# Performance work log

Hardware: AMD Instinct MI355X
Metric: run time of the kernel (lower is better)

## Reference

```python
import jax, jax.numpy as jnp
import numpy as np
import math

DIM_IN = 512
DIM_OUT = 512
KERNEL = 3
STYLE_DIM = 2 * 128
LIN_SCALE = 1.0 / math.sqrt(STYLE_DIM)      # EqualLinear scale (lr_mul=1)
CONV_SCALE = 1.0 / math.sqrt(DIM_IN * KERNEL ** 2)  # fan_in = dim_in * k**2 (as in source)
PAD = KERNEL // 2


def setup_inputs() -> dict:
    key = jax.random.key(0)
    ks = jax.random.split(key, 5)
    B, T = 16, 2048
    x = jax.random.normal(ks[0], (B, DIM_IN, T), dtype=jnp.float32)
    c_src = jax.random.normal(ks[1], (B, 128), dtype=jnp.float32)
    c_trg = jax.random.normal(ks[2], (B, 128), dtype=jnp.float32)
    style_w = jax.random.normal(ks[3], (DIM_IN, STYLE_DIM), dtype=jnp.float32)
    style_b = jnp.ones((DIM_IN,), dtype=jnp.float32)  # bias_init=1
    weight = jax.random.normal(ks[4], (1, DIM_OUT, DIM_IN, KERNEL), dtype=jnp.float32)
    return {"x": x, "c_src": c_src, "c_trg": c_trg,
            "style_w": style_w, "style_b": style_b, "weight": weight}


def reference(x, c_src, c_trg, style_w, style_b, weight):
    B = x.shape[0]
    # EqualLinear: style code s [B, dim_in]
    c = jnp.concatenate([c_src, c_trg], axis=-1)              # [B, 256]
    s = c @ (style_w * LIN_SCALE).T + style_b                 # [B, dim_in]
    # Modulate: w [B, dim_out, dim_in, k]
    w = CONV_SCALE * weight * s[:, None, :, None]
    # Demodulate over (dim_in, k)
    demod = jax.lax.rsqrt(jnp.sum(w * w, axis=(2, 3)) + 1e-8)  # [B, dim_out]
    w = w * demod[:, :, None, None]
    # Per-sample conv1d, padding 'same' (pad = k//2), vmapped over batch
    def conv1(xi, wi):
        # xi: [dim_in, T], wi: [dim_out, dim_in, k]
        out = jax.lax.conv_general_dilated(
            xi[None], wi, window_strides=(1,), padding=[(PAD, PAD)],
            dimension_numbers=("NCH", "OIH", "NCH"))
        return out[0]                                          # [dim_out, T]
    return jax.vmap(conv1)(x, w)                               # [B, dim_out, T]
```

## Files before the change

kernel.cpp:

```cpp
#include <hip/hip_runtime.h>
#include <cstdint>
#include <cstddef>


#define LIN_SCALE  0.0625f
#define CONV_SCALE 0.014731391f

#define B_   16
#define CIN  512
#define COUT 512
#define T_   2048
#define TP   2050

typedef __bf16 bf16x8 __attribute__((ext_vector_type(8)));
typedef float  f32x4  __attribute__((ext_vector_type(4)));
typedef unsigned short u16x8 __attribute__((ext_vector_type(8)));
typedef unsigned short u16x2 __attribute__((ext_vector_type(2)));

#define AS1 __attribute__((address_space(1)))
#define AS3 __attribute__((address_space(3)))

__device__ inline unsigned short f2bf(float f) {
  __bf16 h = (__bf16)f;
  return __builtin_bit_cast(unsigned short, h);
}

__global__ __launch_bounds__(256) void style_kernel(const float* __restrict__ c_src,
                                                    const float* __restrict__ c_trg,
                                                    const float* __restrict__ sw,
                                                    const float* __restrict__ sb,
                                                    float* __restrict__ s) {
  __shared__ float c[256];
  const int b = blockIdx.y;
  const int tid = threadIdx.x;
  c[tid] = (tid < 128) ? c_src[b * 128 + tid] : c_trg[b * 128 + tid - 128];
  __syncthreads();
  const int w = tid >> 6, lane = tid & 63;
  #pragma unroll
  for (int rr = 0; rr < 16; ++rr) {
    const int i = blockIdx.x * 64 + w * 16 + rr;
    const float* row = sw + (size_t)i * 256;
    float acc = row[lane] * c[lane] + row[lane + 64] * c[lane + 64]
              + row[lane + 128] * c[lane + 128] + row[lane + 192] * c[lane + 192];
    #pragma unroll
    for (int off = 32; off; off >>= 1) acc += __shfl_down(acc, off, 64);
    if (lane == 0) s[b * 512 + i] = acc * LIN_SCALE + sb[i];
  }
}

__global__ __launch_bounds__(256) void fused_prep_kernel(const float* __restrict__ x,
                                                         const float* __restrict__ s,
                                                         const float* __restrict__ weight,
                                                         unsigned short* __restrict__ xT,
                                                         float* __restrict__ demod,
                                                         unsigned short* __restrict__ Wb) {
  __shared__ __align__(16) char smem[16896];
  const int id  = blockIdx.x;
  const int tid = threadIdx.x;

  if (id < 4096) {
    float* tile = (float*)smem;
    float* ss   = (float*)(smem + 16640);
    const int t0 = (id & 31) * 64;
    const int i0 = ((id >> 5) & 7) * 64;
    const int b  = id >> 8;

    if (tid < 64) ss[tid] = s[(size_t)b * 512 + i0 + tid];

    const int lr = tid >> 4;
    const int lc = (tid & 15) * 4;
    const float* xb = x + ((size_t)b * CIN + i0) * T_ + t0;
    #pragma unroll
    for (int p = 0; p < 4; ++p) {
      const int r = p * 16 + lr;
      const float4 v = *(const float4*)(xb + (size_t)r * T_ + lc);
      tile[r * 65 + lc + 0] = v.x; tile[r * 65 + lc + 1] = v.y;
      tile[r * 65 + lc + 2] = v.z; tile[r * 65 + lc + 3] = v.w;
    }
    if (t0 == 0 && tid < 8)
      *(u16x8*)&xT[(size_t)b * TP * CIN + i0 + tid * 8] = (u16x8){0,0,0,0,0,0,0,0};
    if (t0 == T_ - 64 && tid < 8)
      *(u16x8*)&xT[((size_t)b * TP + TP - 1) * CIN + i0 + tid * 8] = (u16x8){0,0,0,0,0,0,0,0};
    __syncthreads();

    const int st = tid >> 3;
    const int si = (tid & 7) * 8;
    float sv[8];
    #pragma unroll
    for (int q = 0; q < 8; ++q) sv[q] = ss[si + q];
    unsigned short* xTb = xT + ((size_t)b * TP + 1 + t0) * CIN + i0;
    #pragma unroll
    for (int p = 0; p < 2; ++p) {
      const int t = p * 32 + st;
      u16x8 v;
      #pragma unroll
      for (int q = 0; q < 8; ++q) v[q] = f2bf(tile[(si + q) * 65 + t] * sv[q]);
      *(u16x8*)&xTb[(size_t)t * CIN + si] = v;
    }
  } else {
    const int o = id - 4096;
    float* wsh     = (float*)smem;
    float* partial = (float*)(smem + 6144);

    #pragma unroll
    for (int j = tid; j < 384; j += 256)
      ((float4*)wsh)[j] = ((const float4*)(weight + (size_t)o * 1536))[j];
    __syncthreads();

    float wr[6];
    #pragma unroll
    for (int q = 0; q < 6; ++q) wr[q] = wsh[tid * 6 + q] * CONV_SCALE;

    #pragma unroll
    for (int k = 0; k < 3; ++k) {
      u16x2 v;
      v.x = f2bf(wr[k]);
      v.y = f2bf(wr[3 + k]);
      *(u16x2*)&Wb[((size_t)(k * 512 + o)) * 512 + 2 * tid] = v;
    }

    float s0v[16], s1v[16];
    #pragma unroll
    for (int b = 0; b < 16; ++b) {
      s0v[b] = s[b * 512 + 2 * tid];
      s1v[b] = s[b * 512 + 2 * tid + 1];
    }

    const int lane = tid & 63, w = tid >> 6;
    float ssb[16];
    #pragma unroll
    for (int b = 0; b < 16; ++b) {
      float ssq = 0.f;
      #pragma unroll
      for (int q = 0; q < 3; ++q) { float v = wr[q] * s0v[b]; ssq += v * v; }
      #pragma unroll
      for (int q = 3; q < 6; ++q) { float v = wr[q] * s1v[b]; ssq += v * v; }
      ssb[b] = ssq;
    }
    #pragma unroll
    for (int b = 0; b < 16; ++b) {
      float ssq = ssb[b];
      #pragma unroll
      for (int off = 32; off; off >>= 1) ssq += __shfl_down(ssq, off, 64);
      if (lane == 0) partial[b * 4 + w] = ssq;
    }
    __syncthreads();
    if (tid < 16)
      demod[(size_t)tid * 512 + o] =
          rsqrtf(partial[tid * 4] + partial[tid * 4 + 1] + partial[tid * 4 + 2]
               + partial[tid * 4 + 3] + 1e-8f);
  }
}

__global__ __launch_bounds__(256, 2) void gemm_kernel(const unsigned short* __restrict__ Wb,
                                                      const unsigned short* __restrict__ xT,
                                                      const float* __restrict__ demod,
                                                      float* __restrict__ out) {
  __shared__ unsigned short lA[3 * 128 * 32];
  __shared__ unsigned short lB[258 * 32];

  const int id  = blockIdx.x;
  const int xcd = id & 7;
  const int j   = id >> 3;
  const int b   = xcd + 8 * (j >> 5);
  const int r   = j & 31;
  const int o0  = (r >> 3) * 128;
  const int t0  = (r & 7) * 256;

  const int tid  = threadIdx.x;
  const int lane = tid & 63;
  const int wm   = ((tid >> 6) & 1) * 64;
  const int wn   = (tid >> 7) * 128;
  const int rl   = lane & 15;
  const int kc   = lane >> 4;

  const unsigned short* gW = Wb + (size_t)o0 * 512;
  const unsigned short* gX = xT + ((size_t)b * TP + t0) * CIN;

  f32x4 acc[8][4];
  #pragma unroll
  for (int i = 0; i < 8; ++i)
    #pragma unroll
    for (int jj = 0; jj < 4; ++jj) acc[i][jj] = (f32x4){0.f, 0.f, 0.f, 0.f};

  for (int kk = 0; kk < 16; ++kk) {
    const int i0 = kk * 32;
    __syncthreads();
    #pragma unroll
    for (int q = 0; q < 6; ++q) {
      const int ci  = q * 256 + tid;
      const int row = ci >> 2;
      const int tap = row >> 7;
      const int ar  = row & 127;
      const int gc  = ((ci & 3) ^ ((ar >> 1) & 3)) * 8;
      __builtin_amdgcn_global_load_lds(
          (const AS1 void*)(gW + (size_t)tap * 262144 + (size_t)ar * 512 + i0 + gc),
          (AS3 void*)(&lA[ci * 8]), 16, 0, 0);
    }
    #pragma unroll
    for (int q = 0; q < 4; ++q) {
      const int ci  = q * 256 + tid;
      const int row = ci >> 2;
      const int gc  = ((ci & 3) ^ ((row >> 1) & 3)) * 8;
      __builtin_amdgcn_global_load_lds(
          (const AS1 void*)(gX + (size_t)row * CIN + i0 + gc),
          (AS3 void*)(&lB[ci * 8]), 16, 0, 0);
    }
    if (tid < 8) {
      const int ci  = 1024 + tid;
      const int row = ci >> 2;
      const int gc  = ((ci & 3) ^ ((row >> 1) & 3)) * 8;
      __builtin_amdgcn_global_load_lds(
          (const AS1 void*)(gX + (size_t)row * CIN + i0 + gc),
          (AS3 void*)(&lB[ci * 8]), 16, 0, 0);
    }
    __syncthreads();

    #pragma unroll
    for (int tap = 0; tap < 3; ++tap) {
      bf16x8 wf[4], xf[8];
      #pragma unroll
      for (int ni = 0; ni < 4; ++ni) {
        const int ra = wm + ni * 16 + rl;
        wf[ni] = *(const bf16x8*)&lA[((tap * 128 + ra) * 4 + (kc ^ ((ra >> 1) & 3))) * 8];
      }
      #pragma unroll
      for (int mi = 0; mi < 8; ++mi) {
        const int rb = wn + mi * 16 + rl + tap;
        xf[mi] = *(const bf16x8*)&lB[(rb * 4 + (kc ^ ((rb >> 1) & 3))) * 8];
      }
      #pragma unroll
      for (int mi = 0; mi < 8; ++mi)
        #pragma unroll
        for (int ni = 0; ni < 4; ++ni)
          acc[mi][ni] = __builtin_amdgcn_mfma_f32_16x16x32_bf16(xf[mi], wf[ni], acc[mi][ni], 0, 0, 0);
    }
  }

  const int ccol = lane & 15;
  const int trow = (lane >> 4) * 4;
  float dmv[4];
  #pragma unroll
  for (int ni = 0; ni < 4; ++ni)
    dmv[ni] = demod[(size_t)b * 512 + o0 + wm + ni * 16 + ccol];
  float* ob = out + ((size_t)b * COUT + o0 + wm + ccol) * T_ + t0 + wn + trow;
  #pragma unroll
  for (int mi = 0; mi < 8; ++mi)
    #pragma unroll
    for (int ni = 0; ni < 4; ++ni) {
      f32x4 v = acc[mi][ni];
      v.x *= dmv[ni]; v.y *= dmv[ni]; v.z *= dmv[ni]; v.w *= dmv[ni];
      *(f32x4*)&ob[(size_t)ni * 16 * T_ + mi * 16] = v;
    }
}

extern "C" void kernel_launch(void* const* d_in, const int* in_sizes, int n_in,
                              void* d_out, int out_size, void* d_ws, size_t ws_size,
                              hipStream_t stream) {
  const float* x       = (const float*)d_in[0];
  const float* c_src   = (const float*)d_in[1];
  const float* c_trg   = (const float*)d_in[2];
  const float* style_w = (const float*)d_in[3];
  const float* style_b = (const float*)d_in[4];
  const float* weight  = (const float*)d_in[5];
  float* out = (float*)d_out;

  char* ws = (char*)d_ws;
  float* s_buf          = (float*)ws;
  float* demod_buf      = (float*)(ws + 32768);
  unsigned short* Wb    = (unsigned short*)(ws + 65536);
  unsigned short* xTbuf = (unsigned short*)(ws + 65536 + 1572864);

  style_kernel<<<dim3(8, 16), 256, 0, stream>>>(c_src, c_trg, style_w, style_b, s_buf);
  fused_prep_kernel<<<dim3(4608), 256, 0, stream>>>(x, s_buf, weight, xTbuf,
                                                    demod_buf, Wb);
  gemm_kernel<<<dim3(512), 256, 0, stream>>>(Wb, xTbuf, demod_buf, out);
}
```

Before: 181.3 us.

## Fuse style linear into prep kernel, recomputing style per block

Drops the separate style_kernel launch. The x-transpose blocks and new demod blocks each recompute the style vector they need from c and style_w. X-transpose blocks now each cover 256 time steps over four 64-step iterations, so the style slice is computed once per 256 steps rather than per 64. Demod is computed by 64 separate blocks, one per batch and 128-output chunk, each reading the weight rows and all 512 style values. This removes a launch and a dependency stage in exchange for redundant style GEMV work and more weight reads.

```diff
diff --git a/kernel.cpp b/kernel.cpp
--- a/kernel.cpp
+++ b/kernel.cpp
@@ -25,92 +25,92 @@
   return __builtin_bit_cast(unsigned short, h);
 }
 
-__global__ __launch_bounds__(256) void style_kernel(const float* __restrict__ c_src,
-                                                    const float* __restrict__ c_trg,
-                                                    const float* __restrict__ sw,
-                                                    const float* __restrict__ sb,
-                                                    float* __restrict__ s) {
-  __shared__ float c[256];
-  const int b = blockIdx.y;
-  const int tid = threadIdx.x;
-  c[tid] = (tid < 128) ? c_src[b * 128 + tid] : c_trg[b * 128 + tid - 128];
-  __syncthreads();
-  const int w = tid >> 6, lane = tid & 63;
-  #pragma unroll
-  for (int rr = 0; rr < 16; ++rr) {
-    const int i = blockIdx.x * 64 + w * 16 + rr;
-    const float* row = sw + (size_t)i * 256;
-    float acc = row[lane] * c[lane] + row[lane + 64] * c[lane + 64]
-              + row[lane + 128] * c[lane + 128] + row[lane + 192] * c[lane + 192];
-    #pragma unroll
-    for (int off = 32; off; off >>= 1) acc += __shfl_down(acc, off, 64);
-    if (lane == 0) s[b * 512 + i] = acc * LIN_SCALE + sb[i];
-  }
-}
-
 __global__ __launch_bounds__(256) void fused_prep_kernel(const float* __restrict__ x,
-                                                         const float* __restrict__ s,
+                                                         const float* __restrict__ c_src,
+                                                         const float* __restrict__ c_trg,
+                                                         const float* __restrict__ sw,
+                                                         const float* __restrict__ sb,
                                                          const float* __restrict__ weight,
                                                          unsigned short* __restrict__ xT,
                                                          float* __restrict__ demod,
                                                          unsigned short* __restrict__ Wb) {
-  __shared__ __align__(16) char smem[16896];
+  __shared__ __align__(16) char smem[18944];
   const int id  = blockIdx.x;
   const int tid = threadIdx.x;
 
-  if (id < 4096) {
-    float* tile = (float*)smem;
-    float* ss   = (float*)(smem + 16640);
-    const int t0 = (id & 31) * 64;
-    const int i0 = ((id >> 5) & 7) * 64;
-    const int b  = id >> 8;
-
-    if (tid < 64) ss[tid] = s[(size_t)b * 512 + i0 + tid];
+  if (id < 1024) {
+    float* tile    = (float*)smem;
+    float* c_lds   = (float*)(smem + 16640);
+    float* partial = (float*)(smem + 17664);
+    float* ss      = (float*)(smem + 18688);
+    const int b   = id >> 6;
+    const int i0  = ((id >> 3) & 7) * 64;
+    const int t0b = (id & 7) * 256;
+
+    c_lds[tid] = (tid < 128) ? c_src[b * 128 + tid] : c_trg[b * 128 + tid - 128];
+    __syncthreads();
+    {
+      const int il = tid & 63, q = tid >> 6;
+      const f32x4* swr = (const f32x4*)(sw + (size_t)(i0 + il) * 256 + q * 64);
+      const f32x4* cq  = (const f32x4*)(c_lds + q * 64);
+      float p = 0.f;
+      #pragma unroll
+      for (int j = 0; j < 16; ++j) {
+        const f32x4 wv = swr[j], cv = cq[j];
+        p += wv.x * cv.x + wv.y * cv.y + wv.z * cv.z + wv.w * cv.w;
+      }
+      partial[q * 64 + il] = p;
+    }
+    __syncthreads();
+    if (tid < 64)
+      ss[tid] = LIN_SCALE * (partial[tid] + partial[64 + tid] + partial[128 + tid]
+                           + partial[192 + tid]) + sb[i0 + tid];
+    if (t0b == 0 && tid < 8)
+      *(u16x8*)&xT[(size_t)b * TP * CIN + i0 + tid * 8] = (u16x8){0,0,0,0,0,0,0,0};
+    if (t0b == T_ - 256 && tid < 8)
+      *(u16x8*)&xT[((size_t)b * TP + TP - 1) * CIN + i0 + tid * 8] = (u16x8){0,0,0,0,0,0,0,0};
+    __syncthreads();
 
     const int lr = tid >> 4;
     const int lc = (tid & 15) * 4;
-    const float* xb = x + ((size_t)b * CIN + i0) * T_ + t0;
-    #pragma unroll
-    for (int p = 0; p < 4; ++p) {
-      const int r = p * 16 + lr;
-      const float4 v = *(const float4*)(xb + (size_t)r * T_ + lc);
-      tile[r * 65 + lc + 0] = v.x; tile[r * 65 + lc + 1] = v.y;
-      tile[r * 65 + lc + 2] = v.z; tile[r * 65 + lc + 3] = v.w;
-    }
-    if (t0 == 0 && tid < 8)
-      *(u16x8*)&xT[(size_t)b * TP * CIN + i0 + tid * 8] = (u16x8){0,0,0,0,0,0,0,0};
-    if (t0 == T_ - 64 && tid < 8)
-      *(u16x8*)&xT[((size_t)b * TP + TP - 1) * CIN + i0 + tid * 8] = (u16x8){0,0,0,0,0,0,0,0};
-    __syncthreads();
-
     const int st = tid >> 3;
     const int si = (tid & 7) * 8;
     float sv[8];
     #pragma unroll
     for (int q = 0; q < 8; ++q) sv[q] = ss[si + q];
-    unsigned short* xTb = xT + ((size_t)b * TP + 1 + t0) * CIN + i0;
-    #pragma unroll
-    for (int p = 0; p < 2; ++p) {
-      const int t = p * 32 + st;
-      u16x8 v;
-      #pragma unroll
-      for (int q = 0; q < 8; ++q) v[q] = f2bf(tile[(si + q) * 65 + t] * sv[q]);
-      *(u16x8*)&xTb[(size_t)t * CIN + si] = v;
-    }
-  } else {
-    const int o = id - 4096;
-    float* wsh     = (float*)smem;
-    float* partial = (float*)(smem + 6144);
-
+
+    for (int u = 0; u < 4; ++u) {
+      const int t0 = t0b + u * 64;
+      const float* xb = x + ((size_t)b * CIN + i0) * T_ + t0;
+      #pragma unroll
+      for (int p = 0; p < 4; ++p) {
+        const int r = p * 16 + lr;
+        const float4 v = *(const float4*)(xb + (size_t)r * T_ + lc);
+        tile[r * 65 + lc + 0] = v.x; tile[r * 65 + lc + 1] = v.y;
+        tile[r * 65 + lc + 2] = v.z; tile[r * 65 + lc + 3] = v.w;
+      }
+      __syncthreads();
+      unsigned short* xTb = xT + ((size_t)b * TP + 1 + t0) * CIN + i0;
+      #pragma unroll
+      for (int p = 0; p < 2; ++p) {
+        const int t = p * 32 + st;
+        u16x8 v;
+        #pragma unroll
+        for (int q = 0; q < 8; ++q) v[q] = f2bf(tile[(si + q) * 65 + t] * sv[q]);
+        *(u16x8*)&xTb[(size_t)t * CIN + si] = v;
+      }
+      __syncthreads();
+    }
+  } else if (id < 1536) {
+    const int o = id - 1024;
+    float* wsh = (float*)smem;
     #pragma unroll
     for (int j = tid; j < 384; j += 256)
       ((float4*)wsh)[j] = ((const float4*)(weight + (size_t)o * 1536))[j];
     __syncthreads();
-
     float wr[6];
     #pragma unroll
     for (int q = 0; q < 6; ++q) wr[q] = wsh[tid * 6 + q] * CONV_SCALE;
-
     #pragma unroll
     for (int k = 0; k < 3; ++k) {
       u16x2 v;
@@ -118,37 +118,57 @@
       v.y = f2bf(wr[3 + k]);
       *(u16x2*)&Wb[((size_t)(k * 512 + o)) * 512 + 2 * tid] = v;
     }
-
-    float s0v[16], s1v[16];
-    #pragma unroll
-    for (int b = 0; b < 16; ++b) {
-      s0v[b] = s[b * 512 + 2 * tid];
-      s1v[b] = s[b * 512 + 2 * tid + 1];
-    }
-
-    const int lane = tid & 63, w = tid >> 6;
-    float ssb[16];
-    #pragma unroll
-    for (int b = 0; b < 16; ++b) {
-      float ssq = 0.f;
-      #pragma unroll
-      for (int q = 0; q < 3; ++q) { float v = wr[q] * s0v[b]; ssq += v * v; }
-      #pragma unroll
-      for (int q = 3; q < 6; ++q) { float v = wr[q] * s1v[b]; ssq += v * v; }
-      ssb[b] = ssq;
-    }
-    #pragma unroll
-    for (int b = 0; b < 16; ++b) {
-      float ssq = ssb[b];
-      #pragma unroll
-      for (int off = 32; off; off >>= 1) ssq += __shfl_down(ssq, off, 64);
-      if (lane == 0) partial[b * 4 + w] = ssq;
-    }
-    __syncthreads();
-    if (tid < 16)
-      demod[(size_t)tid * 512 + o] =
-          rsqrtf(partial[tid * 4] + partial[tid * 4 + 1] + partial[tid * 4 + 2]
-               + partial[tid * 4 + 3] + 1e-8f);
+  } else {
+    const int idx = id - 1536;
+    const int b = idx >> 2;
+    const int obase = (idx & 3) * 128;
+    float* c_lds = (float*)smem;
+    float* s_lds = (float*)(smem + 1024);
+
+    c_lds[tid] = (tid < 128) ? c_src[b * 128 + tid] : c_trg[b * 128 + tid - 128];
+    __syncthreads();
+    #pragma unroll
+    for (int h = 0; h < 2; ++h) {
+      const int i = h * 256 + tid;
+      const f32x4* swr = (const f32x4*)(sw + (size_t)i * 256);
+      const f32x4* cv4 = (const f32x4*)c_lds;
+      float acc = 0.f;
+      #pragma unroll 16
+      for (int j = 0; j < 64; ++j) {
+        const f32x4 wv = swr[j], cv = cv4[j];
+        acc += wv.x * cv.x + wv.y * cv.y + wv.z * cv.z + wv.w * cv.w;
+      }
+      s_lds[i] = LIN_SCALE * acc + sb[i];
+    }
+    __syncthreads();
+    const int o = obase + (tid >> 1);
+    const int half = tid & 1;
+    const f32x4* wrow = (const f32x4*)(weight + (size_t)o * 1536 + half * 768);
+    const float* sh = s_lds + half * 256;
+    float ssq = 0.f;
+    #pragma unroll 8
+    for (int ii = 0; ii < 64; ++ii) {
+      const f32x4 a = wrow[ii * 3 + 0];
+      const f32x4 bq = wrow[ii * 3 + 1];
+      const f32x4 c4 = wrow[ii * 3 + 2];
+      const float s0 = sh[ii * 4 + 0], s1 = sh[ii * 4 + 1];
+      const float s2 = sh[ii * 4 + 2], s3 = sh[ii * 4 + 3];
+      float v;
+      v = CONV_SCALE * a.x  * s0; ssq += v * v;
+      v = CONV_SCALE * a.y  * s0; ssq += v * v;
+      v = CONV_SCALE * a.z  * s0; ssq += v * v;
+      v = CONV_SCALE * a.w  * s1; ssq += v * v;
+      v = CONV_SCALE * bq.x * s1; ssq += v * v;
+      v = CONV_SCALE * bq.y * s1; ssq += v * v;
+      v = CONV_SCALE * bq.z * s2; ssq += v * v;
+      v = CONV_SCALE * bq.w * s2; ssq += v * v;
+      v = CONV_SCALE * c4.x * s2; ssq += v * v;
+      v = CONV_SCALE * c4.y * s3; ssq += v * v;
+      v = CONV_SCALE * c4.z * s3; ssq += v * v;
+      v = CONV_SCALE * c4.w * s3; ssq += v * v;
+    }
+    ssq += __shfl_xor(ssq, 1, 64);
+    if (half == 0) demod[(size_t)b * 512 + o] = rsqrtf(ssq + 1e-8f);
   }
 }
 
@@ -266,13 +286,12 @@
   float* out = (float*)d_out;
 
   char* ws = (char*)d_ws;
-  float* s_buf          = (float*)ws;
   float* demod_buf      = (float*)(ws + 32768);
   unsigned short* Wb    = (unsigned short*)(ws + 65536);
   unsigned short* xTbuf = (unsigned short*)(ws + 65536 + 1572864);
 
-  style_kernel<<<dim3(8, 16), 256, 0, stream>>>(c_src, c_trg, style_w, style_b, s_buf);
-  fused_prep_kernel<<<dim3(4608), 256, 0, stream>>>(x, s_buf, weight, xTbuf,
+  fused_prep_kernel<<<dim3(1600), 256, 0, stream>>>(x, c_src, c_trg, style_w,
+                                                    style_b, weight, xTbuf,
                                                     demod_buf, Wb);
   gemm_kernel<<<dim3(512), 256, 0, stream>>>(Wb, xTbuf, demod_buf, out);
 }
```

After: 209.1 us. +15.3%, slower.
